# Performance work log

Hardware: AMD Instinct MI355X
Metric: run time of the kernel (lower is better)

## Reference

```python
import jax, jax.numpy as jnp
import numpy as np

DIM = 1024
MEM = 512
HEAD = DIM // 2


def setup_inputs() -> dict:
    key = jax.random.key(0)
    k0, k1, k2, k3, k4 = jax.random.split(key, 5)
    x = jax.random.normal(k0, (4, 8192, DIM), dtype=jnp.float32)
    keys_real = jax.random.normal(k1, (MEM, HEAD), dtype=jnp.float32) * 0.02
    keys_imag = jax.random.normal(k2, (MEM, HEAD), dtype=jnp.float32) * 0.02
    values_real = jax.random.normal(k3, (MEM, HEAD), dtype=jnp.float32) * 0.02
    values_imag = jax.random.normal(k4, (MEM, HEAD), dtype=jnp.float32) * 0.02
    return {"x": x, "keys_real": keys_real, "keys_imag": keys_imag,
            "values_real": values_real, "values_imag": values_imag}


def reference(x, keys_real, keys_imag, values_real, values_imag):
    input_shape = x.shape
    temperature = HEAD ** (-0.5)
    x_flat = x.reshape(-1, DIM)                       # [N, dim]
    q, p = jnp.split(x_flat, 2, axis=-1)              # each [N, head]
    # dual real/imag score matmuls summed -> energy [N, mem]
    energy = jnp.einsum('nh,mh->nm', q, keys_real) + jnp.einsum('nh,mh->nm', p, keys_imag)
    attn = jax.nn.softmax(energy * temperature, axis=-1)
    out_real = jnp.einsum('nm,mh->nh', attn, values_real)
    out_imag = jnp.einsum('nm,mh->nh', attn, values_imag)
    return jnp.concatenate([out_real, out_imag], axis=-1).reshape(input_shape)
```

## Files before the change

kernel.cpp:

```cpp
#include <hip/hip_runtime.h>


#define DIMX   1024
#define MEMN   512
#define NROWS  32768
#define TEMP   0.04419417382415922f

typedef __bf16 bf16;
typedef __bf16 bf16x8 __attribute__((ext_vector_type(8)));
typedef float  f32x4  __attribute__((ext_vector_type(4)));

__device__ __forceinline__ void gload_lds16(const void* g, void* l) {
    __builtin_amdgcn_global_load_lds(
        (const __attribute__((address_space(1))) unsigned*)g,
        (__attribute__((address_space(3))) unsigned*)l,
        16, 0, 0);
}
__device__ __forceinline__ void gl_b16x8(bf16x8& d, const bf16* p) {
    asm volatile("global_load_dwordx4 %0, %1, off" : "=v"(d) : "v"(p));
}
__device__ __forceinline__ void gl_f32x4(f32x4& d, const float* p) {
    asm volatile("global_load_dwordx4 %0, %1, off" : "=v"(d) : "v"(p));
}
#define VMW(N)     do { asm volatile("s_waitcnt vmcnt(" #N ")" ::: "memory"); \
                        __builtin_amdgcn_sched_barrier(0); } while (0)
#define WAITBAR(N) do { asm volatile("s_waitcnt vmcnt(" #N ") lgkmcnt(0)\n\t" \
                        "s_barrier" ::: "memory");                            \
                        __builtin_amdgcn_sched_barrier(0); } while (0)

__global__ __launch_bounds__(256) void pack_kv_kernel(const float* __restrict__ kr,
                                                      const float* __restrict__ ki,
                                                      const float* __restrict__ vr,
                                                      const float* __restrict__ vi,
                                                      bf16* __restrict__ Kb,
                                                      bf16* __restrict__ Vb) {
    const int idx = blockIdx.x * 256 + threadIdx.x;
    const int e = idx & 7, l = (idx >> 3) & 63;
    const int lm = l & 15, g = l >> 4;
    {
        const int t = (idx >> 9) & 31, c = idx >> 14;
        const int row = t * 16 + lm, k = c * 32 + g * 8 + e;
        const float v = (k < 512) ? kr[row * 512 + k] : ki[row * 512 + (k - 512)];
        Kb[idx] = (bf16)v;
    }
    {
        const int t = (idx >> 9) & 63, c = idx >> 15;
        const int h = t * 16 + lm, m = c * 32 + g * 8 + e;
        const float v = (h < 512) ? vr[m * 512 + h] : vi[m * 512 + (h - 512)];
        Vb[idx] = (bf16)v;
    }
}

__global__ __launch_bounds__(256, 2) void energy_softmax_kernel(
        const float* __restrict__ x,
        const bf16*  __restrict__ Kb,
        bf16* __restrict__ attn) {
    __shared__ __align__(16) bf16 Xs[2][64 * 32];
    __shared__ float red[64][4][2];

    const int tid  = threadIdx.x;
    const int wv   = tid >> 6, lane = tid & 63;
    const int lm   = lane & 15, g = lane >> 4;
    const int rowB = blockIdx.x * 64;

    const int sr = tid >> 2, sc = tid & 3;
    const float* xsrc = x + (size_t)(rowB + sr) * DIMX + sc * 8;
    const int xw_off = sr * 64 + ((sc ^ ((sr >> 1) & 3)) << 4);

    const bf16* kbase = Kb + (wv * 8) * 512 + lane * 8;

    f32x4 acc[4][8] = {};
    f32x4 xa, xb;
    bf16x8 bA[8], bB[8];

#define K_PREF(DST, C) { _Pragma("unroll") for (int j = 0; j < 8; ++j)         \
        gl_b16x8(DST[j], kbase + (size_t)(C) * 16384 + j * 512); }
#define X_PREF(S) { gl_f32x4(xa, xsrc + (S) * 32);                             \
                    gl_f32x4(xb, xsrc + (S) * 32 + 4); }
#define X_WR(B) { bf16x8 w;                                                    \
    w[0]=(bf16)xa[0]; w[1]=(bf16)xa[1]; w[2]=(bf16)xa[2]; w[3]=(bf16)xa[3];    \
    w[4]=(bf16)xb[0]; w[5]=(bf16)xb[1]; w[6]=(bf16)xb[2]; w[7]=(bf16)xb[3];    \
    *(bf16x8*)((char*)Xs[B] + xw_off) = w; }
#define COMPUTE_E(XB, BF) { bf16x8 af[4];                                      \
    _Pragma("unroll") for (int i = 0; i < 4; ++i) { const int r = i * 16 + lm; \
        af[i] = *(const bf16x8*)((const char*)Xs[XB] + r * 64                  \
                                 + ((g ^ ((r >> 1) & 3)) << 4)); }             \
    _Pragma("unroll") for (int i = 0; i < 4; ++i)                              \
        _Pragma("unroll") for (int j = 0; j < 8; ++j)                          \
            acc[i][j] = __builtin_amdgcn_mfma_f32_16x16x32_bf16(               \
                af[i], BF[j], acc[i][j], 0, 0, 0); }

    X_PREF(0);
    K_PREF(bA, 0);
    VMW(8);  X_WR(0);
    X_PREF(1);
    WAITBAR(2);

    for (int t = 0; t < 30; t += 2) {
        K_PREF(bB, t + 1);
        COMPUTE_E(0, bA);
        VMW(8);  X_WR(1);
        X_PREF(t + 2);
        WAITBAR(2);
        K_PREF(bA, t + 2);
        COMPUTE_E(1, bB);
        VMW(8);  X_WR(0);
        X_PREF(t + 3);
        WAITBAR(2);
    }
    K_PREF(bB, 31);
    COMPUTE_E(0, bA);
    VMW(8);  X_WR(1);
    WAITBAR(0);
    COMPUTE_E(1, bB);

#undef K_PREF
#undef X_PREF
#undef X_WR
#undef COMPUTE_E

    float fac[4][4];
    #pragma unroll
    for (int i = 0; i < 4; ++i) {
        #pragma unroll
        for (int rg = 0; rg < 4; ++rg) {
            float m = acc[i][0][rg] * TEMP;
            #pragma unroll
            for (int j = 1; j < 8; ++j) m = fmaxf(m, acc[i][j][rg] * TEMP);
            m = fmaxf(m, __shfl_xor(m, 1));
            m = fmaxf(m, __shfl_xor(m, 2));
            m = fmaxf(m, __shfl_xor(m, 4));
            m = fmaxf(m, __shfl_xor(m, 8));
            float s = 0.f;
            #pragma unroll
            for (int j = 0; j < 8; ++j) {
                const float v = __expf(acc[i][j][rg] * TEMP - m);
                acc[i][j][rg] = v;
                s += v;
            }
            s += __shfl_xor(s, 1);
            s += __shfl_xor(s, 2);
            s += __shfl_xor(s, 4);
            s += __shfl_xor(s, 8);
            const int rr = i * 16 + g * 4 + rg;
            if (lm == 0) { red[rr][wv][0] = m; red[rr][wv][1] = s; }
            fac[i][rg] = m;
        }
    }
    __syncthreads();
    #pragma unroll
    for (int i = 0; i < 4; ++i) {
        #pragma unroll
        for (int rg = 0; rg < 4; ++rg) {
            const int rr = i * 16 + g * 4 + rg;
            const float m0 = red[rr][0][0], s0 = red[rr][0][1];
            const float m1 = red[rr][1][0], s1 = red[rr][1][1];
            const float m2 = red[rr][2][0], s2 = red[rr][2][1];
            const float m3 = red[rr][3][0], s3 = red[rr][3][1];
            const float M  = fmaxf(fmaxf(m0, m1), fmaxf(m2, m3));
            const float S  = s0 * __expf(m0 - M) + s1 * __expf(m1 - M)
                           + s2 * __expf(m2 - M) + s3 * __expf(m3 - M);
            fac[i][rg] = __expf(fac[i][rg] - M) / S;
        }
    }
    #pragma unroll
    for (int i = 0; i < 4; ++i) {
        #pragma unroll
        for (int rg = 0; rg < 4; ++rg) {
            const size_t rr = (size_t)(rowB + i * 16 + g * 4 + rg);
            bf16* p = attn + rr * MEMN + wv * 128 + lm;
            const float f = fac[i][rg];
            #pragma unroll
            for (int j = 0; j < 8; ++j)
                p[j * 16] = (bf16)(acc[i][j][rg] * f);
        }
    }
}

__global__ __launch_bounds__(256, 3) void gemm2_kernel(const bf16* __restrict__ A,
                                                       const bf16* __restrict__ Vb,
                                                       float* __restrict__ C) {
    __shared__ __align__(16) bf16 As[2][128 * 32];

    const int cpx = gridDim.x >> 3;
    const int l   = ((int)blockIdx.x & 7) * cpx + ((int)blockIdx.x >> 3);
    const int bx  = l & 7, by = l >> 3;

    const int tid  = threadIdx.x;
    const int wave = tid >> 6, lane = tid & 63;
    const int lm   = lane & 15, g = lane >> 4;
    const int rowB = by * 128;
    const int wrow = (wave >> 1) * 64;

    const bf16* vbase = Vb + (bx * 8 + (wave & 1) * 4) * 512 + lane * 8;

    f32x4 acc[4][4] = {};
    bf16x8 bA[4], bB[4];

#define STAGE_A(B, C0) { _Pragma("unroll") for (int li = 0; li < 2; ++li) {     \
        const int q = wave * 2 + li;                                            \
        const int r = q * 16 + (lane >> 2);                                     \
        const int ch = lane & 3;                                                \
        gload_lds16(A + (size_t)(rowB + r) * 512 + (C0) * 32                    \
                      + ((ch ^ ((r >> 1) & 3)) << 3),                           \
                    (char*)As[B] + q * 1024); } }
#define B_PREF(DST, C0) { _Pragma("unroll") for (int j = 0; j < 4; ++j)         \
        gl_b16x8(DST[j], vbase + (size_t)(C0) * 32768 + j * 512); }
#define COMPUTE_G(XB, BF) { bf16x8 af[4];                                       \
    _Pragma("unroll") for (int i = 0; i < 4; ++i) {                             \
        const int r = wrow + i * 16 + lm;                                       \
        af[i] = *(const bf16x8*)((const char*)As[XB] + r * 64                   \
                                 + ((g ^ ((r >> 1) & 3)) << 4)); }              \
    _Pragma("unroll") for (int i = 0; i < 4; ++i)                               \
        _Pragma("unroll") for (int j = 0; j < 4; ++j)                           \
            acc[i][j] = __builtin_amdgcn_mfma_f32_16x16x32_bf16(                \
                af[i], BF[j], acc[i][j], 0, 0, 0); }

    STAGE_A(0, 0);
    B_PREF(bA, 0);
    WAITBAR(0);
    for (int t = 0; t < 14; t += 2) {
        STAGE_A(1, t + 1); B_PREF(bB, t + 1); COMPUTE_G(0, bA); WAITBAR(0);
        STAGE_A(0, t + 2); B_PREF(bA, t + 2); COMPUTE_G(1, bB); WAITBAR(0);
    }
    STAGE_A(1, 15); B_PREF(bB, 15); COMPUTE_G(0, bA); WAITBAR(0);
    COMPUTE_G(1, bB);

#undef STAGE_A
#undef B_PREF
#undef COMPUTE_G

    const int r0 = rowB + wrow + g * 4;
    const int c0 = bx * 128 + (wave & 1) * 64 + lm;
    #pragma unroll
    for (int i = 0; i < 4; ++i) {
        #pragma unroll
        for (int j = 0; j < 4; ++j) {
            #pragma unroll
            for (int r = 0; r < 4; ++r)
                C[(size_t)(r0 + i * 16 + r) * DIMX + (c0 + j * 16)] = acc[i][j][r];
        }
    }
}

extern "C" void kernel_launch(void* const* d_in, const int* in_sizes, int n_in,
                              void* d_out, int out_size, void* d_ws, size_t ws_size,
                              hipStream_t stream) {
    const float* x  = (const float*)d_in[0];
    const float* kr = (const float*)d_in[1];
    const float* ki = (const float*)d_in[2];
    const float* vr = (const float*)d_in[3];
    const float* vi = (const float*)d_in[4];
    float* out = (float*)d_out;

    char* ws = (char*)d_ws;
    bf16* Kb   = (bf16*)ws;
    bf16* Vb   = (bf16*)(ws + 1048576);
    bf16* attn = (bf16*)(ws + 2097152);

    pack_kv_kernel<<<2048, 256, 0, stream>>>(kr, ki, vr, vi, Kb, Vb);
    energy_softmax_kernel<<<512, 256, 0, stream>>>(x, Kb, attn);
    gemm2_kernel<<<2048, 256, 0, stream>>>(attn, Vb, out);
}
```

Measured before the change: 292.8 us.

## Deepen GEMM2 LDS ring to four stages and raise MFMA wave priority

gemm2 now uses a four-buffer LDS ring for A tiles, staged two k-steps ahead. Each step has one barrier with a relaxed vmcnt wait instead of a full drain after every step. Both GEMMs wrap their MFMA blocks in s_setprio(1)/s_setprio(0), and gemm1's waits are loosened so the next K fragment loads stay in flight during compute. The larger LDS footprint comes with launch bounds dropping from 3 to 2 blocks per CU, which trades occupancy for more in-flight memory per block.

```diff
diff --git a/kernel.cpp b/kernel.cpp
--- a/kernel.cpp
+++ b/kernel.cpp
@@ -25,6 +25,9 @@
 #define VMW(N)     do { asm volatile("s_waitcnt vmcnt(" #N ")" ::: "memory"); \
                         __builtin_amdgcn_sched_barrier(0); } while (0)
 #define WAITBAR(N) do { asm volatile("s_waitcnt vmcnt(" #N ") lgkmcnt(0)\n\t" \
+                        "s_barrier" ::: "memory");                            \
+                        __builtin_amdgcn_sched_barrier(0); } while (0)
+#define VMWBAR(N)  do { asm volatile("s_waitcnt vmcnt(" #N ")\n\t"            \
                         "s_barrier" ::: "memory");                            \
                         __builtin_amdgcn_sched_barrier(0); } while (0)
 
@@ -71,7 +74,7 @@
 
     f32x4 acc[4][8] = {};
     f32x4 xa, xb;
-    bf16x8 bA[8], bB[8];
+    bf16x8 kf0[8], kf1[8];
 
 #define K_PREF(DST, C) { _Pragma("unroll") for (int j = 0; j < 8; ++j)         \
         gl_b16x8(DST[j], kbase + (size_t)(C) * 16384 + j * 512); }
@@ -81,43 +84,49 @@
     w[0]=(bf16)xa[0]; w[1]=(bf16)xa[1]; w[2]=(bf16)xa[2]; w[3]=(bf16)xa[3];    \
     w[4]=(bf16)xb[0]; w[5]=(bf16)xb[1]; w[6]=(bf16)xb[2]; w[7]=(bf16)xb[3];    \
     *(bf16x8*)((char*)Xs[B] + xw_off) = w; }
-#define COMPUTE_E(XB, BF) { bf16x8 af[4];                                      \
+#define COMPUTE_E(XB, KF) { bf16x8 af[4];                                      \
     _Pragma("unroll") for (int i = 0; i < 4; ++i) { const int r = i * 16 + lm; \
         af[i] = *(const bf16x8*)((const char*)Xs[XB] + r * 64                  \
                                  + ((g ^ ((r >> 1) & 3)) << 4)); }             \
+    __builtin_amdgcn_s_setprio(1);                                             \
     _Pragma("unroll") for (int i = 0; i < 4; ++i)                              \
         _Pragma("unroll") for (int j = 0; j < 8; ++j)                          \
             acc[i][j] = __builtin_amdgcn_mfma_f32_16x16x32_bf16(               \
-                af[i], BF[j], acc[i][j], 0, 0, 0); }
+                af[i], KF[j], acc[i][j], 0, 0, 0);                             \
+    __builtin_amdgcn_s_setprio(0); }
+#define STEP_E(KCUR, KNXT, XB, CH_K, CH_X)                                     \
+    K_PREF(KNXT, CH_K);                                   \
+    VMW(10);                              \
+    COMPUTE_E(XB, KCUR);                                                       \
+    VMW(8);                                                 \
+    X_WR((XB) ^ 1);                                                           \
+    X_PREF(CH_X);                                         \
+    WAITBAR(10);
 
     X_PREF(0);
-    K_PREF(bA, 0);
+    K_PREF(kf0, 0);
     VMW(8);  X_WR(0);
     X_PREF(1);
-    WAITBAR(2);
+    WAITBAR(10);
 
     for (int t = 0; t < 30; t += 2) {
-        K_PREF(bB, t + 1);
-        COMPUTE_E(0, bA);
-        VMW(8);  X_WR(1);
-        X_PREF(t + 2);
-        WAITBAR(2);
-        K_PREF(bA, t + 2);
-        COMPUTE_E(1, bB);
-        VMW(8);  X_WR(0);
-        X_PREF(t + 3);
-        WAITBAR(2);
-    }
-    K_PREF(bB, 31);
-    COMPUTE_E(0, bA);
-    VMW(8);  X_WR(1);
-    WAITBAR(0);
-    COMPUTE_E(1, bB);
+        STEP_E(kf0, kf1, 0, t + 1, t + 2);
+        STEP_E(kf1, kf0, 1, t + 2, t + 3);
+    }
+    K_PREF(kf1, 31);
+    VMW(10);
+    COMPUTE_E(0, kf0);
+    VMW(8);
+    X_WR(1);
+    WAITBAR(8);
+    VMW(0);
+    COMPUTE_E(1, kf1);
 
 #undef K_PREF
 #undef X_PREF
 #undef X_WR
 #undef COMPUTE_E
+#undef STEP_E
 
     float fac[4][4];
     #pragma unroll
@@ -177,10 +186,10 @@
     }
 }
 
-__global__ __launch_bounds__(256, 3) void gemm2_kernel(const bf16* __restrict__ A,
+__global__ __launch_bounds__(256, 2) void gemm2_kernel(const bf16* __restrict__ A,
                                                        const bf16* __restrict__ Vb,
                                                        float* __restrict__ C) {
-    __shared__ __align__(16) bf16 As[2][128 * 32];
+    __shared__ __align__(16) bf16 As[4][128 * 32];
 
     const int cpx = gridDim.x >> 3;
     const int l   = ((int)blockIdx.x & 7) * cpx + ((int)blockIdx.x >> 3);
@@ -195,40 +204,53 @@
     const bf16* vbase = Vb + (bx * 8 + (wave & 1) * 4) * 512 + lane * 8;
 
     f32x4 acc[4][4] = {};
-    bf16x8 bA[4], bB[4];
-
-#define STAGE_A(B, C0) { _Pragma("unroll") for (int li = 0; li < 2; ++li) {     \
+    bf16x8 bf0[4], bf1[4];
+
+#define A_STAGE(BI, C0) { _Pragma("unroll") for (int li = 0; li < 2; ++li) {    \
         const int q = wave * 2 + li;                                            \
         const int r = q * 16 + (lane >> 2);                                     \
         const int ch = lane & 3;                                                \
         gload_lds16(A + (size_t)(rowB + r) * 512 + (C0) * 32                    \
                       + ((ch ^ ((r >> 1) & 3)) << 3),                           \
-                    (char*)As[B] + q * 1024); } }
+                    (char*)As[BI] + q * 1024); } }
 #define B_PREF(DST, C0) { _Pragma("unroll") for (int j = 0; j < 4; ++j)         \
         gl_b16x8(DST[j], vbase + (size_t)(C0) * 32768 + j * 512); }
-#define COMPUTE_G(XB, BF) { bf16x8 af[4];                                       \
+#define COMPUTE_G(BI, BF) { bf16x8 af[4];                                       \
     _Pragma("unroll") for (int i = 0; i < 4; ++i) {                             \
         const int r = wrow + i * 16 + lm;                                       \
-        af[i] = *(const bf16x8*)((const char*)As[XB] + r * 64                   \
+        af[i] = *(const bf16x8*)((const char*)As[BI] + r * 64                   \
                                  + ((g ^ ((r >> 1) & 3)) << 4)); }              \
+    __builtin_amdgcn_s_setprio(1);                                              \
     _Pragma("unroll") for (int i = 0; i < 4; ++i)                               \
         _Pragma("unroll") for (int j = 0; j < 4; ++j)                           \
             acc[i][j] = __builtin_amdgcn_mfma_f32_16x16x32_bf16(                \
-                af[i], BF[j], acc[i][j], 0, 0, 0); }
-
-    STAGE_A(0, 0);
-    B_PREF(bA, 0);
-    WAITBAR(0);
+                af[i], BF[j], acc[i][j], 0, 0, 0);                              \
+    __builtin_amdgcn_s_setprio(0); }
+#define STEP_G(BCUR, BNXT, T)                                                   \
+    A_STAGE((T + 2) & 3, T + 2);                     \
+    B_PREF(BNXT, T + 1);                                             \
+    VMW(6);                             \
+    VMWBAR(6);                        \
+    COMPUTE_G((T) & 3, BCUR);
+
+    A_STAGE(0, 0);
+    A_STAGE(1, 1);
+    B_PREF(bf0, 0);
     for (int t = 0; t < 14; t += 2) {
-        STAGE_A(1, t + 1); B_PREF(bB, t + 1); COMPUTE_G(0, bA); WAITBAR(0);
-        STAGE_A(0, t + 2); B_PREF(bA, t + 2); COMPUTE_G(1, bB); WAITBAR(0);
-    }
-    STAGE_A(1, 15); B_PREF(bB, 15); COMPUTE_G(0, bA); WAITBAR(0);
-    COMPUTE_G(1, bB);
-
-#undef STAGE_A
+        STEP_G(bf0, bf1, t);
+        STEP_G(bf1, bf0, t + 1);
+    }
+    B_PREF(bf1, 15);
+    VMW(4);
+    VMWBAR(4);
+    COMPUTE_G(2, bf0);
+    VMW(0);
+    COMPUTE_G(3, bf1);
+
+#undef A_STAGE
 #undef B_PREF
 #undef COMPUTE_G
+#undef STEP_G
 
     const int r0 = rowB + wrow + g * 4;
     const int c0 = bx * 128 + (wave & 1) * 64 + lm;
```

Result: no change. 291.5 us (-0.5%).
